# Kernel optimization log

Measured on AMD Instinct MI355X. Metric: run time of the kernel, lower is better.

The kernel has to match this reference:

```python
import jax, jax.numpy as jnp
import numpy as np

B, G, N_IN, N_HID, N_OUT = 2, 4096, 8, 32, 32
ALPHA, BETA, BN_EPS = 0.005, 5e-5, 1e-5
EDGE_P = 0.05  # adjacency density


def _lin_init(k, fan_in, fan_out):
    k1, k2 = jax.random.split(k)
    lim = 1.0 / np.sqrt(fan_in)
    W = jax.random.uniform(k1, (fan_in, fan_out), minval=-lim, maxval=lim, dtype=jnp.float32)
    b = jax.random.uniform(k2, (fan_out,), minval=-lim, maxval=lim, dtype=jnp.float32)
    return W, b


def setup_inputs() -> dict:
    key = jax.random.key(0)
    ks = jax.random.split(key, 12)
    W_infer, b_infer = _lin_init(ks[0], N_IN, N_HID)
    W_e1, b_e1 = _lin_init(ks[1], 2 * N_HID, 1)
    W_e2, b_e2 = _lin_init(ks[2], 2 * N_HID, 1)
    W_n1, b_n1 = _lin_init(ks[3], 2 * N_HID, N_OUT)
    W_n2, b_n2 = _lin_init(ks[4], 2 * N_HID, N_OUT)
    W_m1, b_m1 = _lin_init(ks[5], 2 * N_HID, N_OUT)
    W_m2, b_m2 = _lin_init(ks[6], 2 * N_HID, N_OUT)
    x = jax.random.normal(ks[7], (B, G, N_IN), dtype=jnp.float32)
    edges1 = jax.random.bernoulli(ks[8], EDGE_P, (G, G)).astype(jnp.float32)
    edges2 = jax.random.bernoulli(ks[9], EDGE_P, (G, G)).astype(jnp.float32)
    bn_gamma = jnp.ones((G,), jnp.float32)
    bn_beta = jnp.zeros((G,), jnp.float32)
    return dict(x=x, edges1=edges1, edges2=edges2, W_infer=W_infer, b_infer=b_infer,
                W_e1=W_e1, b_e1=b_e1, W_e2=W_e2, b_e2=b_e2,
                W_n1=W_n1, b_n1=b_n1, W_n2=W_n2, b_n2=b_n2,
                W_m1=W_m1, b_m1=b_m1, W_m2=W_m2, b_m2=b_m2,
                bn_gamma=bn_gamma, bn_beta=bn_beta)


def _mp_block(x, adj, coef, W_e, b_e, W_n, b_n, W_m, b_m):
    # x: [B,G,H]. Torch builds edge feature at flat index k=i*G+j as cat([x_j, x_i])
    # (shape2 = col gather, shape1 = row gather). We keep the same math without
    # materializing the [B,G*G,2H] tensor.
    Hh = x.shape[-1]
    s_src = x @ W_e[:Hh]   # [B,G,1]  (x_j part of mlp_edge)
    s_dst = x @ W_e[Hh:]   # [B,G,1]  (x_i part of mlp_edge)
    logits = s_dst[:, :, None, 0] + s_src[:, None, :, 0] + b_e[0]   # [B,G,G] at (i,j)
    w = adj + coef * (adj == 0).astype(x.dtype)                     # ori_edge + coef*thres_edge
    e = jax.nn.sigmoid(logits) * w[None]                            # [B,G,G]
    # receive at node i: sum_j e_ij * [x_j, x_i]
    recv_src = jnp.einsum('bij,bjh->bih', e, x)                     # sum_j e_ij x_j
    recv_dst = x * jnp.sum(e, axis=2)[..., None]                    # x_i * sum_j e_ij
    recv = jnp.concatenate([recv_src, recv_dst], axis=-1)           # [B,G,2H]
    recv = jax.nn.elu(recv @ W_n + b_n)                             # nodes_mlp + elu
    upd = jnp.concatenate([recv, x], axis=-1) @ W_m + b_m           # mesg_merge (mode='cat')
    return jax.nn.elu(upd)


def _forward(x, edges1, edges2, W_infer, b_infer, W_e1, b_e1, W_e2, b_e2,
             W_n1, b_n1, W_n2, b_n2, W_m1, b_m1, W_m2, b_m2, bn_gamma, bn_beta):
    h = jax.nn.elu(x @ W_infer + b_infer)                           # infer + elu, [B,G,H]
    h = _mp_block(h, edges1, ALPHA, W_e1, b_e1, W_n1, b_n1, W_m1, b_m1)
    # BatchNorm1d(gene_num) on [B, G, n_out]: per-gene stats over (batch, feature)
    mu = jnp.mean(h, axis=(0, 2), keepdims=True)
    var = jnp.var(h, axis=(0, 2), keepdims=True)
    h = (h - mu) * jax.lax.rsqrt(var + BN_EPS)
    h = h * bn_gamma[None, :, None] + bn_beta[None, :, None]
    return _mp_block(h, edges2, BETA, W_e2, b_e2, W_n2, b_n2, W_m2, b_m2)


def reference(x, edges1, edges2, W_infer, b_infer, W_e1, b_e1, W_e2, b_e2,
              W_n1, b_n1, W_n2, b_n2, W_m1, b_m1, W_m2, b_m2, bn_gamma, bn_beta):
    return _forward(x, edges1, edges2, W_infer, b_infer, W_e1, b_e1, W_e2, b_e2,
                    W_n1, b_n1, W_n2, b_n2, W_m1, b_m1, W_m2, b_m2, bn_gamma, bn_beta)
```

## Files before the change

kernel.cpp:

```cpp
#include <hip/hip_runtime.h>

#define G 4096
#define BSZ 2
#define NIN 8
#define HID 32
#define NLOG2E (-1.4426950408889634f)

typedef __attribute__((ext_vector_type(8))) short short8;
typedef __attribute__((ext_vector_type(4))) float floatx4;
typedef unsigned short ushort_t;
typedef unsigned int uint_t;

__device__ __forceinline__ float elu1(float v) {
    return v > 0.f ? v : (__expf(v) - 1.f);
}
__device__ __forceinline__ ushort_t f2bf(float f) {
    unsigned u = __float_as_uint(f);
    u += 0x7fffu + ((u >> 16) & 1u);
    return (ushort_t)(u >> 16);
}

__global__ __launch_bounds__(256) void k_setup1(
    const float* __restrict__ x, const float* __restrict__ W,
    const float* __restrict__ bias, const float* __restrict__ We,
    float* __restrict__ h0, ushort_t* __restrict__ hTb,
    float* __restrict__ ssrc, float* __restrict__ sdst) {
    __shared__ __align__(16) ushort_t hs[HID][264];
    int tid = threadIdx.x;
    int t = blockIdx.x * 256 + tid;
    int b = t >> 12;
    int g0 = (blockIdx.x & 15) * 256;
    float xin[NIN];
    const float* xp = x + t * NIN;
#pragma unroll
    for (int k = 0; k < NIN; k++) xin[k] = xp[k];
    float ss = 0.f, sd = 0.f;
    float* hp = h0 + (size_t)t * HID;
#pragma unroll
    for (int o = 0; o < HID; o++) {
        float v = bias[o];
#pragma unroll
        for (int k = 0; k < NIN; k++) v += xin[k] * W[k * HID + o];
        v = elu1(v);
        hp[o] = v;
        hs[o][tid] = f2bf(v);
        ss += v * We[o];
        sd += v * We[HID + o];
    }
    ssrc[t] = ss * NLOG2E;
    sdst[t] = sd * NLOG2E;
    __syncthreads();
#pragma unroll
    for (int p = 0; p < 4; p++) {
        int row = p * 8 + (tid >> 5);
        int c = (tid & 31) * 8;
        short8 v8 = *(const short8*)&hs[row][c];
        *(short8*)(void*)&hTb[(size_t)(b * HID + row) * G + g0 + c] = v8;
    }
}

template <bool DO_BN>
__global__ __launch_bounds__(1024, 4) void k_fused(
    const float* __restrict__ adj, const float* __restrict__ ssrc,
    const float* __restrict__ sdst, const ushort_t* __restrict__ hTb_in,
    const float* __restrict__ bep, float coef, const float* __restrict__ hin,
    const float* __restrict__ Wn, const float* __restrict__ bnb,
    const float* __restrict__ Wm, const float* __restrict__ bmb,
    const float* __restrict__ gamma, const float* __restrict__ beta,
    const float* __restrict__ We2, float* __restrict__ outp,
    ushort_t* __restrict__ hTb_out, float* __restrict__ s2s,
    float* __restrict__ s2d) {
    __shared__ __align__(16) float red[14][64][9];
    __shared__ __align__(16) float rec[32][68];
    __shared__ __align__(16) float rec2[32][68];
    __shared__ __align__(16) float esg[16][2];
    __shared__ __align__(16) ushort_t tbuf[BSZ][HID][16];
    __shared__ __align__(16) float Wns[2048];
    __shared__ __align__(16) float Wms[2048];

    int tid = threadIdx.x;
    int g0 = blockIdx.x * 16;
    int l = tid & 63, w = tid >> 6;
    int b = w >> 3, jq = w & 7;

    if (tid < 512) {
        ((float4*)Wns)[tid] = ((const float4*)Wn)[tid];
    } else {
        int t2 = tid - 512;
        ((float4*)Wms)[t2] = ((const float4*)Wm)[t2];
    }

    int m = l & 15, kg = l >> 4;
    float sd2 = sdst[b * G + g0 + m] + bep[0] * NLOG2E;
    int jstart = jq * 512;
    const ushort_t* hb0 = hTb_in + (size_t)(b * HID + m) * G + jstart + kg * 8;
    const ushort_t* hb1 = hb0 + (size_t)16 * G;
    const float* ap = adj + (size_t)(g0 + m) * G + jstart + kg * 8;
    const float* sp = ssrc + b * G + jstart + kg * 8;
    floatx4 c0 = {0.f, 0.f, 0.f, 0.f}, c1 = {0.f, 0.f, 0.f, 0.f};
    float es = 0.f;
    short8 pb0[2], pb1[2];
    float4 av0[2], av1[2];
#pragma unroll
    for (int d = 0; d < 2; d++) {
        pb0[d] = *(const short8*)(const void*)(hb0 + d * 32);
        pb1[d] = *(const short8*)(const void*)(hb1 + d * 32);
        av0[d] = *(const float4*)(ap + d * 32);
        av1[d] = *(const float4*)(ap + d * 32 + 4);
    }

#pragma unroll 4
    for (int jc = 0; jc < 16; jc++) {
        int cur = jc & 1;
        short8 bf0 = pb0[cur], bf1 = pb1[cur];
        float4 a0 = av0[cur], a1 = av1[cur];
        if (jc + 2 < 16) {
            int o = (jc + 2) * 32;
            pb0[cur] = *(const short8*)(const void*)(hb0 + o);
            pb1[cur] = *(const short8*)(const void*)(hb1 + o);
            av0[cur] = *(const float4*)(ap + o);
            av1[cur] = *(const float4*)(ap + o + 4);
        }
        float4 s0 = *(const float4*)(sp + jc * 32);
        float4 s1 = *(const float4*)(sp + jc * 32 + 4);
        float sv[8] = {s0.x, s0.y, s0.z, s0.w, s1.x, s1.y, s1.z, s1.w};
        float avf[8] = {a0.x, a0.y, a0.z, a0.w, a1.x, a1.y, a1.z, a1.w};
        short8 af;
#pragma unroll
        for (int t = 0; t < 8; t++) {
            float v = avf[t];
            float wgt = (v != 0.f) ? v : coef;
            float ex = exp2f(sd2 + sv[t]);
            float e = __builtin_amdgcn_rcpf(1.f + ex) * wgt;
            es += e;
            af[t] = (short)f2bf(e);
        }
        c0 = __builtin_amdgcn_mfma_f32_16x16x32_bf16(af, bf0, c0, 0, 0, 0);
        c1 = __builtin_amdgcn_mfma_f32_16x16x32_bf16(af, bf1, c1, 0, 0, 0);
    }
    if (jq) {
        int widx = b * 7 + jq - 1;
#pragma unroll
        for (int r = 0; r < 4; r++) {
            red[widx][l][r] = c0[r];
            red[widx][l][4 + r] = c1[r];
        }
        red[widx][l][8] = es;
    }
    __syncthreads();
    if (!jq) {
#pragma unroll
        for (int q = 0; q < 7; q++) {
            int widx = b * 7 + q;
#pragma unroll
            for (int r = 0; r < 4; r++) {
                c0[r] += red[widx][l][r];
                c1[r] += red[widx][l][4 + r];
            }
            es += red[widx][l][8];
        }
        es += __shfl_xor(es, 16);
        es += __shfl_xor(es, 32);
#pragma unroll
        for (int r = 0; r < 4; r++) {
            int gene = (l >> 4) * 4 + r;
            rec[gene * 2 + b][m] = c0[r];
            rec[gene * 2 + b][16 + m] = c1[r];
        }
        if (l < 16) esg[l][b] = es;
    }
    __syncthreads();

    int rl = tid >> 5, hh = tid & 31;
    int gene = rl >> 1, bb = rl & 1;
    float xv = hin[((size_t)(bb * G + g0 + gene)) * HID + hh];
    rec[rl][32 + hh] = xv * esg[gene][bb];
    __syncthreads();

    float v = bnb[hh];
#pragma unroll
    for (int k4 = 0; k4 < 16; k4++) {
        float4 r4 = *(const float4*)&rec[rl][k4 * 4];
        v += r4.x * Wns[(k4 * 4 + 0) * HID + hh];
        v += r4.y * Wns[(k4 * 4 + 1) * HID + hh];
        v += r4.z * Wns[(k4 * 4 + 2) * HID + hh];
        v += r4.w * Wns[(k4 * 4 + 3) * HID + hh];
    }
    v = elu1(v);
    rec2[rl][hh] = v;
    rec2[rl][32 + hh] = xv;
    float u = bmb[hh];
#pragma unroll
    for (int k4 = 0; k4 < 16; k4++) {
        float4 r4 = *(const float4*)&rec2[rl][k4 * 4];
        u += r4.x * Wms[(k4 * 4 + 0) * HID + hh];
        u += r4.y * Wms[(k4 * 4 + 1) * HID + hh];
        u += r4.z * Wms[(k4 * 4 + 2) * HID + hh];
        u += r4.w * Wms[(k4 * 4 + 3) * HID + hh];
    }
    float h1v = elu1(u);
    if (!DO_BN) {
        outp[((size_t)(bb * G + g0 + gene)) * HID + hh] = h1v;
    } else {
        float s = h1v, sq = h1v * h1v;
#pragma unroll
        for (int mm = 32; mm; mm >>= 1) {
            s += __shfl_xor(s, mm);
            sq += __shfl_xor(sq, mm);
        }
        float mu = s * (1.f / 64.f);
        float var = sq * (1.f / 64.f) - mu * mu;
        float rstd = rsqrtf(var + 1e-5f);
        float hn = (h1v - mu) * rstd * gamma[g0 + gene] + beta[g0 + gene];
        outp[((size_t)(bb * G + g0 + gene)) * HID + hh] = hn;
        tbuf[bb][hh][gene] = f2bf(hn);
        float ps = hn * We2[hh], pd = hn * We2[HID + hh];
#pragma unroll
        for (int mm = 16; mm; mm >>= 1) {
            ps += __shfl_xor(ps, mm);
            pd += __shfl_xor(pd, mm);
        }
        if (hh == 0) {
            s2s[bb * G + g0 + gene] = ps * NLOG2E;
            s2d[bb * G + g0 + gene] = pd * NLOG2E;
        }
        __syncthreads();
        if (tid < 128) {
            int b2 = tid >> 6, c = (tid >> 1) & 31, half = tid & 1;
            short8 v8 = *(const short8*)&tbuf[b2][c][half * 8];
            *(short8*)(void*)&hTb_out[(size_t)(b2 * HID + c) * G + g0 + half * 8] = v8;
        }
    }
}

extern "C" void kernel_launch(void* const* d_in, const int* in_sizes, int n_in,
                              void* d_out, int out_size, void* d_ws, size_t ws_size,
                              hipStream_t stream) {
    const float* x      = (const float*)d_in[0];
    const float* edges1 = (const float*)d_in[1];
    const float* edges2 = (const float*)d_in[2];
    const float* W_inf  = (const float*)d_in[3];
    const float* b_inf  = (const float*)d_in[4];
    const float* W_e1   = (const float*)d_in[5];
    const float* b_e1   = (const float*)d_in[6];
    const float* W_e2   = (const float*)d_in[7];
    const float* b_e2   = (const float*)d_in[8];
    const float* W_n1   = (const float*)d_in[9];
    const float* b_n1   = (const float*)d_in[10];
    const float* W_n2   = (const float*)d_in[11];
    const float* b_n2   = (const float*)d_in[12];
    const float* W_m1   = (const float*)d_in[13];
    const float* b_m1   = (const float*)d_in[14];
    const float* W_m2   = (const float*)d_in[15];
    const float* b_m2   = (const float*)d_in[16];
    const float* bn_g   = (const float*)d_in[17];
    const float* bn_b   = (const float*)d_in[18];
    float* out = (float*)d_out;

    float* ws = (float*)d_ws;
    float* h0   = ws;
    float* h1n  = ws + 262144;
    float* s1s  = ws + 524288;
    float* s1d  = ws + 532480;
    float* s2s  = ws + 540672;
    float* s2d  = ws + 548864;
    ushort_t* hTb  = (ushort_t*)(ws + 557056);
    ushort_t* hTb2 = (ushort_t*)(ws + 688128);

    const float ALPHA = 0.005f, BETA = 5e-5f;

    k_setup1<<<32, 256, 0, stream>>>(x, W_inf, b_inf, W_e1, h0, hTb, s1s, s1d);
    k_fused<true><<<G / 16, 1024, 0, stream>>>(
        edges1, s1s, s1d, hTb, b_e1, ALPHA, h0, W_n1, b_n1, W_m1, b_m1,
        bn_g, bn_b, W_e2, h1n, hTb2, s2s, s2d);
    k_fused<false><<<G / 16, 1024, 0, stream>>>(
        edges2, s2s, s2d, hTb2, b_e2, BETA, h1n, W_n2, b_n2, W_m2, b_m2,
        nullptr, nullptr, nullptr, out, nullptr, nullptr, nullptr);
}
```

Before: 258.9 us.

## Stage adjacency as shared bitmask so both batch halves share one adj read

```diff
diff --git a/kernel.cpp b/kernel.cpp
--- a/kernel.cpp
+++ b/kernel.cpp
@@ -70,6 +70,7 @@
     const float* __restrict__ We2, float* __restrict__ outp,
     ushort_t* __restrict__ hTb_out, float* __restrict__ s2s,
     float* __restrict__ s2d) {
+    __shared__ __align__(16) uint_t abits[2][32][16];
     __shared__ __align__(16) float red[14][64][9];
     __shared__ __align__(16) float rec[32][68];
     __shared__ __align__(16) float rec2[32][68];
@@ -90,54 +91,99 @@
         ((float4*)Wms)[t2] = ((const float4*)Wm)[t2];
     }
 
+    const int sh = (tid & 7) * 4;
+    const bool st = (tid & 7) == 0;
+    const int jw = (tid & 255) >> 3;
+    const int rbase = tid >> 8;
+    const int joff = (tid & 255) * 4;
+
+#define LOADC(c_, r_)                                                        \
+    {                                                                        \
+        _Pragma("unroll") for (int s = 0; s < 4; s++)                        \
+            r_[s] = *(const float4*)&adj[(size_t)(g0 + s * 4 + rbase) * G +  \
+                                         (c_) * 1024 + joff];                \
+    }
+#define PACKW(buf_, r_)                                                      \
+    {                                                                        \
+        _Pragma("unroll") for (int s = 0; s < 4; s++) {                      \
+            float4 v4 = r_[s];                                               \
+            uint_t nib = (uint_t)(v4.x != 0.f) |                             \
+                         ((uint_t)(v4.y != 0.f) << 1) |                      \
+                         ((uint_t)(v4.z != 0.f) << 2) |                      \
+                         ((uint_t)(v4.w != 0.f) << 3);                       \
+            uint_t wd = nib << sh;                                           \
+            wd |= __shfl_xor(wd, 1);                                         \
+            wd |= __shfl_xor(wd, 2);                                         \
+            wd |= __shfl_xor(wd, 4);                                         \
+            if (st) abits[buf_][jw][s * 4 + rbase] = wd;                     \
+        }                                                                    \
+    }
+
     int m = l & 15, kg = l >> 4;
     float sd2 = sdst[b * G + g0 + m] + bep[0] * NLOG2E;
-    int jstart = jq * 512;
-    const ushort_t* hb0 = hTb_in + (size_t)(b * HID + m) * G + jstart + kg * 8;
+    const float wm1 = 1.f - coef;
+    const ushort_t* hb0 = hTb_in + (size_t)(b * HID + m) * G + jq * 128 + kg * 8;
     const ushort_t* hb1 = hb0 + (size_t)16 * G;
-    const float* ap = adj + (size_t)(g0 + m) * G + jstart + kg * 8;
-    const float* sp = ssrc + b * G + jstart + kg * 8;
+    const float* sp = ssrc + b * G + jq * 128 + kg * 8;
     floatx4 c0 = {0.f, 0.f, 0.f, 0.f}, c1 = {0.f, 0.f, 0.f, 0.f};
     float es = 0.f;
     short8 pb0[2], pb1[2];
-    float4 av0[2], av1[2];
+    float4 sv0[2], sv1[2];
 #pragma unroll
     for (int d = 0; d < 2; d++) {
-        pb0[d] = *(const short8*)(const void*)(hb0 + d * 32);
-        pb1[d] = *(const short8*)(const void*)(hb1 + d * 32);
-        av0[d] = *(const float4*)(ap + d * 32);
-        av1[d] = *(const float4*)(ap + d * 32 + 4);
-    }
-
-#pragma unroll 4
-    for (int jc = 0; jc < 16; jc++) {
-        int cur = jc & 1;
-        short8 bf0 = pb0[cur], bf1 = pb1[cur];
-        float4 a0 = av0[cur], a1 = av1[cur];
-        if (jc + 2 < 16) {
-            int o = (jc + 2) * 32;
-            pb0[cur] = *(const short8*)(const void*)(hb0 + o);
-            pb1[cur] = *(const short8*)(const void*)(hb1 + o);
-            av0[cur] = *(const float4*)(ap + o);
-            av1[cur] = *(const float4*)(ap + o + 4);
-        }
-        float4 s0 = *(const float4*)(sp + jc * 32);
-        float4 s1 = *(const float4*)(sp + jc * 32 + 4);
-        float sv[8] = {s0.x, s0.y, s0.z, s0.w, s1.x, s1.y, s1.z, s1.w};
-        float avf[8] = {a0.x, a0.y, a0.z, a0.w, a1.x, a1.y, a1.z, a1.w};
-        short8 af;
-#pragma unroll
-        for (int t = 0; t < 8; t++) {
-            float v = avf[t];
-            float wgt = (v != 0.f) ? v : coef;
-            float ex = exp2f(sd2 + sv[t]);
-            float e = __builtin_amdgcn_rcpf(1.f + ex) * wgt;
-            es += e;
-            af[t] = (short)f2bf(e);
-        }
-        c0 = __builtin_amdgcn_mfma_f32_16x16x32_bf16(af, bf0, c0, 0, 0, 0);
-        c1 = __builtin_amdgcn_mfma_f32_16x16x32_bf16(af, bf1, c1, 0, 0, 0);
-    }
+        int o = d * 32;
+        pb0[d] = *(const short8*)(const void*)(hb0 + o);
+        pb1[d] = *(const short8*)(const void*)(hb1 + o);
+        sv0[d] = *(const float4*)(sp + o);
+        sv1[d] = *(const float4*)(sp + o + 4);
+    }
+
+    float4 ra[4], rb[4];
+    LOADC(0, ra);
+    PACKW(0, ra);
+    LOADC(1, rb);
+    __syncthreads();
+
+#pragma unroll
+    for (int c = 0; c < 4; ++c) {
+        int cur = c & 1;
+#pragma unroll
+        for (int j2 = 0; j2 < 4; ++j2) {
+            int t = c * 4 + j2;
+            int pc = t & 1;
+            short8 bf0 = pb0[pc], bf1 = pb1[pc];
+            float4 s0 = sv0[pc], s1 = sv1[pc];
+            if (t + 2 < 16) {
+                int o = ((t + 2) >> 2) * 1024 + ((t + 2) & 3) * 32;
+                pb0[pc] = *(const short8*)(const void*)(hb0 + o);
+                pb1[pc] = *(const short8*)(const void*)(hb1 + o);
+                sv0[pc] = *(const float4*)(sp + o);
+                sv1[pc] = *(const float4*)(sp + o + 4);
+            }
+            uint_t bw = abits[cur][jq * 4 + j2][m];
+            float sv[8] = {s0.x, s0.y, s0.z, s0.w, s1.x, s1.y, s1.z, s1.w};
+            short8 af;
+#pragma unroll
+            for (int t8 = 0; t8 < 8; t8++) {
+                float bitf = (float)((bw >> (kg * 8 + t8)) & 1u);
+                float wgt = __builtin_fmaf(bitf, wm1, coef);
+                float ex = exp2f(sd2 + sv[t8]);
+                float e = __builtin_amdgcn_rcpf(1.f + ex) * wgt;
+                es += e;
+                af[t8] = (short)f2bf(e);
+            }
+            c0 = __builtin_amdgcn_mfma_f32_16x16x32_bf16(af, bf0, c0, 0, 0, 0);
+            c1 = __builtin_amdgcn_mfma_f32_16x16x32_bf16(af, bf1, c1, 0, 0, 0);
+        }
+        if (c < 3) {
+            PACKW(cur ^ 1, rb);
+            if (c < 2) LOADC(c + 2, rb);
+        }
+        __syncthreads();
+    }
+#undef LOADC
+#undef PACKW
+
     if (jq) {
         int widx = b * 7 + jq - 1;
 #pragma unroll
```

Measured after the change: 282.7 us. 9.2% more time.
